# Performance work log

Hardware: AMD Instinct MI355X
Metric: run time of the kernel (lower is better)

The kernel has to match this reference:

```python
import jax, jax.numpy as jnp
import numpy as np

D_MODEL = 1024
NUM_HEADS = 16
D_K = D_MODEL // NUM_HEADS


def setup_inputs() -> dict:
    key = jax.random.key(0)
    ks = jax.random.split(key, 11)
    B, S = 2, 2048
    scale = 1.0 / np.sqrt(D_MODEL)
    inp = {
        "q": jax.random.normal(ks[0], (B, S, D_MODEL), jnp.float32),
        "k": jax.random.normal(ks[1], (B, S, D_MODEL), jnp.float32),
        "v": jax.random.normal(ks[2], (B, S, D_MODEL), jnp.float32),
        "wq": jax.random.normal(ks[3], (D_MODEL, D_MODEL), jnp.float32) * scale,
        "bq": jax.random.normal(ks[4], (D_MODEL,), jnp.float32) * 0.01,
        "wk": jax.random.normal(ks[5], (D_MODEL, D_MODEL), jnp.float32) * scale,
        "bk": jax.random.normal(ks[6], (D_MODEL,), jnp.float32) * 0.01,
        "wv": jax.random.normal(ks[7], (D_MODEL, D_MODEL), jnp.float32) * scale,
        "bv": jax.random.normal(ks[8], (D_MODEL,), jnp.float32) * 0.01,
        "wo": jax.random.normal(ks[9], (D_MODEL, D_MODEL), jnp.float32) * scale,
        "bo": jax.random.normal(ks[10], (D_MODEL,), jnp.float32) * 0.01,
    }
    return inp


def reference(q, k, v, wq, bq, wk, bk, wv, bv, wo, bo):
    B, S, _ = q.shape
    # Linear projections (torch Linear: x @ W.T + b). Weights stored [out, in].
    qh = (q @ wq.T + bq).reshape(B, S, NUM_HEADS, D_K).transpose(0, 2, 1, 3)  # [B,H,S,dk]
    kh = (k @ wk.T + bk).reshape(B, S, NUM_HEADS, D_K).transpose(0, 2, 1, 3)
    vh = (v @ wv.T + bv).reshape(B, S, NUM_HEADS, D_K).transpose(0, 2, 1, 3)
    scores = jnp.einsum("bhqd,bhkd->bhqk", qh, kh) / jnp.sqrt(jnp.asarray(D_K, qh.dtype))
    weights = jax.nn.softmax(scores, axis=-1)
    attn = jnp.einsum("bhqk,bhkd->bhqd", weights, vh)  # [B,H,S,dk]
    attn = attn.transpose(0, 2, 1, 3).reshape(B, S, D_MODEL)
    return attn @ wo.T + bo
```

## Files before the change

### kernel.cpp

```cpp
#include <hip/hip_runtime.h>

#define DM 1024
#define NH 16
#define DK 64
#define BB 2
#define SS 2048
#define MT (BB*SS)

typedef __attribute__((ext_vector_type(8))) short bf16x8;
typedef __attribute__((ext_vector_type(4))) float f32x4;

#define QSCALE 0.1803368801111191f
#define EXPC  (-14.426950408889634f)

__device__ __forceinline__ unsigned short f2bf(float f) {
    unsigned int u = __float_as_uint(f);
    u += 0x7FFF + ((u >> 16) & 1);
    return (unsigned short)(u >> 16);
}

__device__ __forceinline__ unsigned int cvt_pk_bf16(float lo, float hi) {
    unsigned int r;
    asm("v_cvt_pk_bf16_f32 %0, %1, %2" : "=v"(r) : "v"(lo), "v"(hi));
    return r;
}

__device__ __forceinline__ void gload16(const void* g, void* l) {
    __builtin_amdgcn_global_load_lds(
        (const __attribute__((address_space(1))) unsigned int*)g,
        (__attribute__((address_space(3))) unsigned int*)(unsigned int)(unsigned long long)l,
        16, 0, 0);
}

__device__ __forceinline__ int kperm(int s) {
    return (s & ~31) | (((s >> 2) & 1) << 4) | (((s >> 3) & 3) << 2) | (s & 3);
}

struct CvtArgs {
    const float* s[4];
    unsigned short* d[4];
    float scl[4];
};

__global__ __launch_bounds__(256) void cvt_f32_bf16(CvtArgs a) {
    const int arr = blockIdx.y;
    const int i = (blockIdx.x * 256 + threadIdx.x) * 8;
    const float sc = a.scl[arr];
    const float4* sp = (const float4*)(a.s[arr] + i);
    float4 x = sp[0], y = sp[1];
    union { unsigned short us[8]; uint4 u4; } r;
    r.us[0] = f2bf(x.x * sc); r.us[1] = f2bf(x.y * sc);
    r.us[2] = f2bf(x.z * sc); r.us[3] = f2bf(x.w * sc);
    r.us[4] = f2bf(y.x * sc); r.us[5] = f2bf(y.y * sc);
    r.us[6] = f2bf(y.z * sc); r.us[7] = f2bf(y.w * sc);
    *(uint4*)(a.d[arr] + i) = r.u4;
}

struct ProjArgs {
    const void* A[3];
    const void* B[3];
    const float* bias[3];
    unsigned short* out[3];
    float bscale[3];
};

__global__ __launch_bounds__(256, 3) void proj3(ProjArgs pa) {
    __shared__ __align__(16) unsigned short As[2][128 * 32];
    __shared__ __align__(16) unsigned short Bs[2][128 * 32];

    const int z = blockIdx.y;
    const int bx = blockIdx.x;
    const int xcd = bx & 7, ib = bx >> 3;
    int mb, nb;
    if (z < 2) { mb = xcd * 4 + (ib >> 3); nb = ib & 7; }
    else       { mb = ib >> 2;             nb = xcd * 4 + (ib & 3); }
    const int m0 = mb * 128, n0 = nb * 128;

    const bool a32 = (z < 2);
    const float* Fsrc = (const float*)(a32 ? pa.A[z] : pa.B[z]);
    const unsigned short* Gsrc = (const unsigned short*)(a32 ? pa.B[z] : pa.A[z]);
    const int f0r = a32 ? m0 : n0;
    const int g0r = a32 ? n0 : m0;
    unsigned short* const Fb[2] = { a32 ? As[0] : Bs[0], a32 ? As[1] : Bs[1] };
    unsigned short* const Gb[2] = { a32 ? Bs[0] : As[0], a32 ? Bs[1] : As[1] };

    const float* bias = pa.bias[z];
    const float bsc = pa.bscale[z];
    unsigned short* out = pa.out[z];

    const int tid = (int)threadIdx.x;
    const int l = tid & 63;
    const int w = tid >> 6;
    const int wm = w >> 1, wn = w & 1;

    const int strow = l >> 2;
    const int sslot = (l & 3) ^ ((l >> 3) & 3);
    const int fr = l & 15, fj = l >> 4;
    const int swz = ((fj ^ ((fr >> 1) & 3)) << 4);

    const f32x4 zero = {0.f, 0.f, 0.f, 0.f};
    f32x4 acc[4][4];
    #pragma unroll
    for (int mf = 0; mf < 4; ++mf)
        #pragma unroll
        for (int nf = 0; nf < 4; ++nf) acc[mf][nf] = zero;

    float4 r0[2][2], r1[2][2];

    #pragma unroll
    for (int t = 0; t < 2; ++t) {
        const int c = w * 2 + t;
        const int row = c * 16 + strow;
        const int col = sslot * 8;
        const float4* s = (const float4*)(Fsrc + (size_t)(f0r + row) * DM + col);
        float4 f0v = s[0], f1v = s[1];
        union { unsigned int u[4]; bf16x8 v; } pk;
        pk.u[0] = cvt_pk_bf16(f0v.x, f0v.y); pk.u[1] = cvt_pk_bf16(f0v.z, f0v.w);
        pk.u[2] = cvt_pk_bf16(f1v.x, f1v.y); pk.u[3] = cvt_pk_bf16(f1v.z, f1v.w);
        *(bf16x8*)((char*)Fb[0] + c * 1024 + l * 16) = pk.v;
        gload16(Gsrc + (size_t)(g0r + row) * DM + col, (char*)Gb[0] + c * 1024);
    }
    #pragma unroll
    for (int t = 0; t < 2; ++t) {
        const int row = (w * 2 + t) * 16 + strow;
        const float4* s = (const float4*)(Fsrc + (size_t)(f0r + row) * DM + 32 + sslot * 8);
        r0[t][0] = s[0]; r0[t][1] = s[1];
    }
    __syncthreads();

    auto body = [&](int k, int cb, float4 (&rin)[2][2], float4 (&rout)[2][2]) {
        if (k + 64 < DM) {
            #pragma unroll
            for (int t = 0; t < 2; ++t) {
                const int row = (w * 2 + t) * 16 + strow;
                const float4* s = (const float4*)(Fsrc + (size_t)(f0r + row) * DM + (k + 64) + sslot * 8);
                rout[t][0] = s[0]; rout[t][1] = s[1];
            }
        }
        if (k + 32 < DM) {
            #pragma unroll
            for (int t = 0; t < 2; ++t) {
                const int c = w * 2 + t;
                const int row = c * 16 + strow;
                gload16(Gsrc + (size_t)(g0r + row) * DM + (k + 32) + sslot * 8, (char*)Gb[cb ^ 1] + c * 1024);
            }
        }
        bf16x8 af[4], bfr[4];
        #pragma unroll
        for (int mf = 0; mf < 4; ++mf)
            af[mf] = *(const bf16x8*)((const char*)As[cb] + (wm * 64 + mf * 16 + fr) * 64 + swz);
        #pragma unroll
        for (int nf = 0; nf < 4; ++nf)
            bfr[nf] = *(const bf16x8*)((const char*)Bs[cb] + (wn * 64 + nf * 16 + fr) * 64 + swz);
        #pragma unroll
        for (int mf = 0; mf < 4; ++mf)
            #pragma unroll
            for (int nf = 0; nf < 4; ++nf)
                acc[mf][nf] = __builtin_amdgcn_mfma_f32_16x16x32_bf16(af[mf], bfr[nf], acc[mf][nf], 0, 0, 0);
        if (k + 32 < DM) {
            #pragma unroll
            for (int t = 0; t < 2; ++t) {
                const int c = w * 2 + t;
                union { unsigned int u[4]; bf16x8 v; } pk;
                pk.u[0] = cvt_pk_bf16(rin[t][0].x, rin[t][0].y);
                pk.u[1] = cvt_pk_bf16(rin[t][0].z, rin[t][0].w);
                pk.u[2] = cvt_pk_bf16(rin[t][1].x, rin[t][1].y);
                pk.u[3] = cvt_pk_bf16(rin[t][1].z, rin[t][1].w);
                *(bf16x8*)((char*)Fb[cb ^ 1] + c * 1024 + l * 16) = pk.v;
            }
        }
        __syncthreads();
    };

    for (int kt = 0; kt < DM; kt += 64) {
        body(kt, 0, r0, r1);
        body(kt + 32, 1, r1, r0);
    }

    #pragma unroll
    for (int nf = 0; nf < 4; ++nf) {
        const int n = n0 + wn * 64 + nf * 16 + fr;
        const float bn = (z == 2) ? 0.f : bias[n] * bsc;
        #pragma unroll
        for (int mf = 0; mf < 4; ++mf) {
            #pragma unroll
            for (int j = 0; j < 4; ++j) {
                const int m = m0 + wm * 64 + mf * 16 + fj * 4 + j;
                if (z < 2) {
                    const float val = acc[mf][nf][j] + bn;
                    int s = m & (SS - 1);
                    if (z == 1) s = kperm(s);
                    out[((size_t)((m >> 11) * NH + (n >> 6)) * SS + s) * DK + (n & 63)] = f2bf(val);
                } else {
                    const float val = acc[mf][nf][j] + bias[m];
                    out[(size_t)((n >> 11) * NH + (m >> 6)) * (SS * DK) + (size_t)(m & 63) * SS + (n & (SS - 1))] = f2bf(val);
                }
            }
        }
    }
}

__global__ __launch_bounds__(256, 2) void gemm_out(
    const unsigned short* __restrict__ A,
    const unsigned short* __restrict__ B,
    const float* __restrict__ bias,
    float* __restrict__ out)
{
    __shared__ __align__(16) unsigned short As[2][128 * 32];
    __shared__ __align__(16) unsigned short Bs[2][64 * 32];

    const int tid = (int)threadIdx.x;
    const int l = tid & 63;
    const int w = tid >> 6;
    const int wm = w >> 1, wn = w & 1;
    const int m0 = blockIdx.x * 128, n0 = blockIdx.y * 64;

    const int strow = l >> 2;
    const int sslot = (l & 3) ^ ((l >> 3) & 3);
    const int fr = l & 15, fj = l >> 4;
    const int swz = ((fj ^ ((fr >> 1) & 3)) << 4);

    const f32x4 zero = {0.f, 0.f, 0.f, 0.f};
    f32x4 acc[4][2];
    #pragma unroll
    for (int mf = 0; mf < 4; ++mf)
        #pragma unroll
        for (int nf = 0; nf < 2; ++nf) acc[mf][nf] = zero;

    #pragma unroll
    for (int t = 0; t < 2; ++t) {
        const int c = w * 2 + t;
        gload16(A + (size_t)(m0 + c * 16 + strow) * DM + sslot * 8, (char*)As[0] + c * 1024);
    }
    gload16(B + (size_t)(n0 + w * 16 + strow) * DM + sslot * 8, (char*)Bs[0] + w * 1024);
    __syncthreads();

    for (int kt = 0; kt < DM; kt += 32) {
        const int cb = (kt >> 5) & 1;
        if (kt + 32 < DM) {
            #pragma unroll
            for (int t = 0; t < 2; ++t) {
                const int c = w * 2 + t;
                gload16(A + (size_t)(m0 + c * 16 + strow) * DM + (kt + 32) + sslot * 8, (char*)As[cb ^ 1] + c * 1024);
            }
            gload16(B + (size_t)(n0 + w * 16 + strow) * DM + (kt + 32) + sslot * 8, (char*)Bs[cb ^ 1] + w * 1024);
        }
        bf16x8 af[4], bfr[2];
        #pragma unroll
        for (int mf = 0; mf < 4; ++mf)
            af[mf] = *(const bf16x8*)((const char*)As[cb] + (wm * 64 + mf * 16 + fr) * 64 + swz);
        #pragma unroll
        for (int nf = 0; nf < 2; ++nf)
            bfr[nf] = *(const bf16x8*)((const char*)Bs[cb] + (wn * 32 + nf * 16 + fr) * 64 + swz);
        #pragma unroll
        for (int mf = 0; mf < 4; ++mf)
            #pragma unroll
            for (int nf = 0; nf < 2; ++nf)
                acc[mf][nf] = __builtin_amdgcn_mfma_f32_16x16x32_bf16(af[mf], bfr[nf], acc[mf][nf], 0, 0, 0);
        __syncthreads();
    }

    #pragma unroll
    for (int nf = 0; nf < 2; ++nf) {
        const int n = n0 + wn * 32 + nf * 16 + fr;
        const float bn = bias[n];
        #pragma unroll
        for (int mf = 0; mf < 4; ++mf)
            #pragma unroll
            for (int j = 0; j < 4; ++j) {
                const int m = m0 + wm * 64 + mf * 16 + fj * 4 + j;
                out[(size_t)m * DM + n] = acc[mf][nf][j] + bn;
            }
    }
}

__global__ __launch_bounds__(256, 2) void attn_bf16(
    const unsigned short* __restrict__ qh,
    const unsigned short* __restrict__ kh,
    const unsigned short* __restrict__ vt,
    unsigned short* __restrict__ ao)
{
    __shared__ __align__(16) unsigned short Ks[2][128 * 64];
    __shared__ __align__(16) unsigned short Vs[2][2][64 * 64];

    const int tid = (int)threadIdx.x;
    const int l = tid & 63;
    const int w = tid >> 6;
    const int bh = blockIdx.x;
    const int q0 = blockIdx.y * 128;
    const size_t pb = (size_t)bh * (SS * DK);

    const int fr = l & 15, fj = l >> 4;
    const int s8 = fr & 7;
    const int strow = l >> 3;
    const int sslot = (l & 7) ^ strow;

    bf16x8 qreg[2][2];
    #pragma unroll
    for (int qf = 0; qf < 2; ++qf)
        #pragma unroll
        for (int ks = 0; ks < 2; ++ks)
            qreg[qf][ks] = *(const bf16x8*)(qh + pb + (size_t)(q0 + w * 32 + qf * 16 + fr) * DK + ks * 32 + fj * 8);

    #pragma unroll
    for (int t = 0; t < 4; ++t) {
        const int c = w * 4 + t;
        gload16(kh + pb + (size_t)(c * 8 + strow) * DK + sslot * 8, (char*)Ks[0] + c * 1024);
    }
    #pragma unroll
    for (int s = 0; s < 2; ++s)
        #pragma unroll
        for (int tt = 0; tt < 2; ++tt) {
            const int ch = w * 2 + tt;
            gload16(vt + pb + (size_t)(ch * 8 + strow) * SS + s * 64 + sslot * 8, (char*)Vs[0][s] + ch * 1024);
        }
    asm volatile("s_waitcnt vmcnt(0)" ::: "memory");
    __syncthreads();

    const f32x4 zero = {0.f, 0.f, 0.f, 0.f};
    f32x4 ot[4][2];
    f32x4 lacc[2];
    #pragma unroll
    for (int nf = 0; nf < 4; ++nf)
        #pragma unroll
        for (int qf = 0; qf < 2; ++qf) ot[nf][qf] = zero;
    lacc[0] = zero; lacc[1] = zero;

    const int NT = SS / 128;
    for (int t = 0; t < NT; ++t) {
        const int c = t & 1;
        if (t + 1 < NT) {
            #pragma unroll
            for (int t4 = 0; t4 < 4; ++t4) {
                const int ch = w * 4 + t4;
                gload16(kh + pb + (size_t)((t + 1) * 128 + ch * 8 + strow) * DK + sslot * 8,
                        (char*)Ks[c ^ 1] + ch * 1024);
            }
        }
        f32x4 sc[8][2];
        #pragma unroll
        for (int kf = 0; kf < 8; ++kf)
            #pragma unroll
            for (int qf = 0; qf < 2; ++qf) sc[kf][qf] = zero;
        __builtin_amdgcn_s_setprio(1);
        #pragma unroll
        for (int ks = 0; ks < 2; ++ks) {
            bf16x8 kfr[8];
            #pragma unroll
            for (int kf = 0; kf < 8; ++kf)
                kfr[kf] = *(const bf16x8*)((const char*)Ks[c] + (kf * 16 + fr) * 128 + (((ks * 4 + fj) ^ s8) << 4));
            #pragma unroll
            for (int kf = 0; kf < 8; ++kf)
                #pragma unroll
                for (int qf = 0; qf < 2; ++qf)
                    sc[kf][qf] = __builtin_amdgcn_mfma_f32_16x16x32_bf16(kfr[kf], qreg[qf][ks], sc[kf][qf], 0, 0, 0);
        }
        __builtin_amdgcn_s_setprio(0);

        bf16x8 pbf[2][4];
        #pragma unroll
        for (int qf = 0; qf < 2; ++qf) {
            #pragma unroll
            for (int kss = 0; kss < 4; ++kss) {
                union { unsigned int u[4]; bf16x8 v; } pk;
                #pragma unroll
                for (int kf = 0; kf < 2; ++kf) {
                    const f32x4 s4 = sc[kss * 2 + kf][qf];
                    const float e0 = __builtin_amdgcn_exp2f(s4[0] + EXPC);
                    const float e1 = __builtin_amdgcn_exp2f(s4[1] + EXPC);
                    const float e2 = __builtin_amdgcn_exp2f(s4[2] + EXPC);
                    const float e3 = __builtin_amdgcn_exp2f(s4[3] + EXPC);
                    lacc[qf][0] += e0; lacc[qf][1] += e1;
                    lacc[qf][2] += e2; lacc[qf][3] += e3;
                    pk.u[kf * 2 + 0] = cvt_pk_bf16(e0, e1);
                    pk.u[kf * 2 + 1] = cvt_pk_bf16(e2, e3);
                }
                pbf[qf][kss] = pk.v;
            }
        }

        __builtin_amdgcn_sched_barrier(0);
        asm volatile("s_waitcnt vmcnt(0) lgkmcnt(0)" ::: "memory");
        __builtin_amdgcn_s_barrier();
        __builtin_amdgcn_sched_barrier(0);

        if (t + 1 < NT) {
            #pragma unroll
            for (int s = 0; s < 2; ++s)
                #pragma unroll
                for (int tt = 0; tt < 2; ++tt) {
                    const int ch = w * 2 + tt;
                    gload16(vt + pb + (size_t)(ch * 8 + strow) * SS + (t + 1) * 128 + s * 64 + sslot * 8,
                            (char*)Vs[c ^ 1][s] + ch * 1024);
                }
        }

        __builtin_amdgcn_s_setprio(1);
        #pragma unroll
        for (int kss = 0; kss < 4; ++kss) {
            const int sub = kss >> 1, kw = kss & 1;
            bf16x8 va[4];
            #pragma unroll
            for (int nf = 0; nf < 4; ++nf)
                va[nf] = *(const bf16x8*)((const char*)Vs[c][sub] + (nf * 16 + fr) * 128 + (((kw * 4 + fj) ^ s8) << 4));
            #pragma unroll
            for (int nf = 0; nf < 4; ++nf)
                #pragma unroll
                for (int qf = 0; qf < 2; ++qf)
                    ot[nf][qf] = __builtin_amdgcn_mfma_f32_16x16x32_bf16(va[nf], pbf[qf][kss], ot[nf][qf], 0, 0, 0);
        }
        __builtin_amdgcn_s_setprio(0);
    }

    float inv[2];
    #pragma unroll
    for (int qf = 0; qf < 2; ++qf) {
        float s = (lacc[qf][0] + lacc[qf][1]) + (lacc[qf][2] + lacc[qf][3]);
        s += __shfl_xor(s, 16);
        s += __shfl_xor(s, 32);
        inv[qf] = 1.0f / s;
    }
    const int b = bh >> 4, h = bh & 15;
    #pragma unroll
    for (int qf = 0; qf < 2; ++qf) {
        const int qg = q0 + w * 32 + qf * 16 + fr;
        unsigned short* dst = ao + (size_t)(b * SS + qg) * DM + h * DK + fj * 4;
        #pragma unroll
        for (int nf = 0; nf < 4; ++nf) {
            uint2 pw;
            pw.x = cvt_pk_bf16(ot[nf][qf][0] * inv[qf], ot[nf][qf][1] * inv[qf]);
            pw.y = cvt_pk_bf16(ot[nf][qf][2] * inv[qf], ot[nf][qf][3] * inv[qf]);
            *(uint2*)(dst + nf * 16) = pw;
        }
    }
}

extern "C" void kernel_launch(void* const* d_in, const int* in_sizes, int n_in,
                              void* d_out, int out_size, void* d_ws, size_t ws_size,
                              hipStream_t stream) {
    const float* q  = (const float*)d_in[0];
    const float* k  = (const float*)d_in[1];
    const float* v  = (const float*)d_in[2];
    const float* wq = (const float*)d_in[3];
    const float* bq = (const float*)d_in[4];
    const float* wk = (const float*)d_in[5];
    const float* bk = (const float*)d_in[6];
    const float* wv = (const float*)d_in[7];
    const float* bv = (const float*)d_in[8];
    const float* wo = (const float*)d_in[9];
    const float* bo = (const float*)d_in[10];

    const size_t NQ = (size_t)MT * DM;
    const size_t NW = (size_t)DM * DM;
    unsigned short* wsb = (unsigned short*)d_ws;
    unsigned short* wqb = wsb;
    unsigned short* wkb = wqb + NW;
    unsigned short* wvb = wkb + NW;
    unsigned short* wob = wvb + NW;
    unsigned short* qhb = wob + NW;
    unsigned short* khb = qhb + NQ;
    unsigned short* vtb = khb + NQ;
    unsigned short* aob = vtb + NQ;

    CvtArgs ca;
    ca.s[0] = wq; ca.d[0] = wqb; ca.scl[0] = QSCALE;
    ca.s[1] = wk; ca.d[1] = wkb; ca.scl[1] = 1.f;
    ca.s[2] = wv; ca.d[2] = wvb; ca.scl[2] = 1.f;
    ca.s[3] = wo; ca.d[3] = wob; ca.scl[3] = 1.f;
    cvt_f32_bf16<<<dim3(512, 4), dim3(256), 0, stream>>>(ca);

    ProjArgs pa;
    pa.A[0] = q;   pa.B[0] = wqb; pa.bias[0] = bq; pa.out[0] = qhb; pa.bscale[0] = QSCALE;
    pa.A[1] = k;   pa.B[1] = wkb; pa.bias[1] = bk; pa.out[1] = khb; pa.bscale[1] = 1.f;
    pa.A[2] = wvb; pa.B[2] = v;   pa.bias[2] = bv; pa.out[2] = vtb; pa.bscale[2] = 1.f;
    proj3<<<dim3(256, 3), dim3(256), 0, stream>>>(pa);

    attn_bf16<<<dim3(32, 16), dim3(256), 0, stream>>>(qhb, khb, vtb, aob);

    gemm_out<<<dim3(32, 16), dim3(256), 0, stream>>>(aob, wob, bo, (float*)d_out);
}
```

Baseline: 112.7 us.

## Triple-buffer direct-to-LDS bf16 operand loads in proj3 with explicit vmcnt waits

The projection GEMM now keeps the bf16 operand, loaded directly into LDS, in a three-stage ring and issues its load two k-steps ahead instead of one. __syncthreads is replaced by an explicit s_waitcnt vmcnt plus s_barrier, so in-flight global loads for later stages are not drained at each barrier. The aim is to hide global memory latency. In exchange LDS use per block grows from 32KB to 40KB, which may reduce occupancy at launch_bounds 3, and the hand-counted vmcnt values are fragile.

```diff
diff --git a/kernel.cpp b/kernel.cpp
--- a/kernel.cpp
+++ b/kernel.cpp
@@ -65,8 +65,8 @@
 };
 
 __global__ __launch_bounds__(256, 3) void proj3(ProjArgs pa) {
-    __shared__ __align__(16) unsigned short As[2][128 * 32];
-    __shared__ __align__(16) unsigned short Bs[2][128 * 32];
+    __shared__ __align__(16) unsigned short Fb[2][128 * 32];
+    __shared__ __align__(16) unsigned short Gr[3][128 * 32];
 
     const int z = blockIdx.y;
     const int bx = blockIdx.x;
@@ -81,8 +81,6 @@
     const unsigned short* Gsrc = (const unsigned short*)(a32 ? pa.B[z] : pa.A[z]);
     const int f0r = a32 ? m0 : n0;
     const int g0r = a32 ? n0 : m0;
-    unsigned short* const Fb[2] = { a32 ? As[0] : Bs[0], a32 ? As[1] : Bs[1] };
-    unsigned short* const Gb[2] = { a32 ? Bs[0] : As[0], a32 ? Bs[1] : As[1] };
 
     const float* bias = pa.bias[z];
     const float bsc = pa.bscale[z];
@@ -107,18 +105,34 @@
 
     float4 r0[2][2], r1[2][2];
 
+    float4 f0v[2][2];
+    #pragma unroll
+    for (int t = 0; t < 2; ++t) {
+        const int row = (w * 2 + t) * 16 + strow;
+        const float4* s = (const float4*)(Fsrc + (size_t)(f0r + row) * DM + sslot * 8);
+        f0v[t][0] = s[0]; f0v[t][1] = s[1];
+    }
     #pragma unroll
     for (int t = 0; t < 2; ++t) {
         const int c = w * 2 + t;
         const int row = c * 16 + strow;
-        const int col = sslot * 8;
-        const float4* s = (const float4*)(Fsrc + (size_t)(f0r + row) * DM + col);
-        float4 f0v = s[0], f1v = s[1];
+        gload16(Gsrc + (size_t)(g0r + row) * DM + sslot * 8, (char*)Gr[0] + c * 1024);
+    }
+    #pragma unroll
+    for (int t = 0; t < 2; ++t) {
+        const int c = w * 2 + t;
+        const int row = c * 16 + strow;
+        gload16(Gsrc + (size_t)(g0r + row) * DM + 32 + sslot * 8, (char*)Gr[1] + c * 1024);
+    }
+    #pragma unroll
+    for (int t = 0; t < 2; ++t) {
+        const int c = w * 2 + t;
         union { unsigned int u[4]; bf16x8 v; } pk;
-        pk.u[0] = cvt_pk_bf16(f0v.x, f0v.y); pk.u[1] = cvt_pk_bf16(f0v.z, f0v.w);
-        pk.u[2] = cvt_pk_bf16(f1v.x, f1v.y); pk.u[3] = cvt_pk_bf16(f1v.z, f1v.w);
+        pk.u[0] = cvt_pk_bf16(f0v[t][0].x, f0v[t][0].y);
+        pk.u[1] = cvt_pk_bf16(f0v[t][0].z, f0v[t][0].w);
+        pk.u[2] = cvt_pk_bf16(f0v[t][1].x, f0v[t][1].y);
+        pk.u[3] = cvt_pk_bf16(f0v[t][1].z, f0v[t][1].w);
         *(bf16x8*)((char*)Fb[0] + c * 1024 + l * 16) = pk.v;
-        gload16(Gsrc + (size_t)(g0r + row) * DM + col, (char*)Gb[0] + c * 1024);
     }
     #pragma unroll
     for (int t = 0; t < 2; ++t) {
@@ -126,38 +140,46 @@
         const float4* s = (const float4*)(Fsrc + (size_t)(f0r + row) * DM + 32 + sslot * 8);
         r0[t][0] = s[0]; r0[t][1] = s[1];
     }
-    __syncthreads();
-
-    auto body = [&](int k, int cb, float4 (&rin)[2][2], float4 (&rout)[2][2]) {
-        if (k + 64 < DM) {
+    __builtin_amdgcn_sched_barrier(0);
+    asm volatile("s_waitcnt vmcnt(4) lgkmcnt(0)" ::: "memory");
+    __builtin_amdgcn_s_barrier();
+    __builtin_amdgcn_sched_barrier(0);
+
+    auto body = [&](int k, int cb, int gcur, int giss,
+                    float4 (&rin)[2][2], float4 (&rout)[2][2]) {
+        const bool pf64 = (k + 64 < DM);
+        const bool pf32 = (k + 32 < DM);
+        if (pf64) {
             #pragma unroll
             for (int t = 0; t < 2; ++t) {
                 const int row = (w * 2 + t) * 16 + strow;
                 const float4* s = (const float4*)(Fsrc + (size_t)(f0r + row) * DM + (k + 64) + sslot * 8);
                 rout[t][0] = s[0]; rout[t][1] = s[1];
             }
-        }
-        if (k + 32 < DM) {
             #pragma unroll
             for (int t = 0; t < 2; ++t) {
                 const int c = w * 2 + t;
                 const int row = c * 16 + strow;
-                gload16(Gsrc + (size_t)(g0r + row) * DM + (k + 32) + sslot * 8, (char*)Gb[cb ^ 1] + c * 1024);
-            }
-        }
+                gload16(Gsrc + (size_t)(g0r + row) * DM + (k + 64) + sslot * 8,
+                        (char*)Gr[0] + giss * 8192 + c * 1024);
+            }
+        }
+        const char* GLds = (const char*)Gr[0] + gcur * 8192;
+        const char* ALds = a32 ? (const char*)Fb[cb] : GLds;
+        const char* BLds = a32 ? GLds : (const char*)Fb[cb];
         bf16x8 af[4], bfr[4];
         #pragma unroll
         for (int mf = 0; mf < 4; ++mf)
-            af[mf] = *(const bf16x8*)((const char*)As[cb] + (wm * 64 + mf * 16 + fr) * 64 + swz);
+            af[mf] = *(const bf16x8*)(ALds + (wm * 64 + mf * 16 + fr) * 64 + swz);
         #pragma unroll
         for (int nf = 0; nf < 4; ++nf)
-            bfr[nf] = *(const bf16x8*)((const char*)Bs[cb] + (wn * 64 + nf * 16 + fr) * 64 + swz);
+            bfr[nf] = *(const bf16x8*)(BLds + (wn * 64 + nf * 16 + fr) * 64 + swz);
         #pragma unroll
         for (int mf = 0; mf < 4; ++mf)
             #pragma unroll
             for (int nf = 0; nf < 4; ++nf)
                 acc[mf][nf] = __builtin_amdgcn_mfma_f32_16x16x32_bf16(af[mf], bfr[nf], acc[mf][nf], 0, 0, 0);
-        if (k + 32 < DM) {
+        if (pf32) {
             #pragma unroll
             for (int t = 0; t < 2; ++t) {
                 const int c = w * 2 + t;
@@ -169,12 +191,18 @@
                 *(bf16x8*)((char*)Fb[cb ^ 1] + c * 1024 + l * 16) = pk.v;
             }
         }
-        __syncthreads();
+        __builtin_amdgcn_sched_barrier(0);
+        if (pf64) asm volatile("s_waitcnt vmcnt(6) lgkmcnt(0)" ::: "memory");
+        else      asm volatile("s_waitcnt vmcnt(0) lgkmcnt(0)" ::: "memory");
+        __builtin_amdgcn_s_barrier();
+        __builtin_amdgcn_sched_barrier(0);
     };
 
+    int s = 0;
     for (int kt = 0; kt < DM; kt += 64) {
-        body(kt, 0, r0, r1);
-        body(kt + 32, 1, r1, r0);
+        body(kt,      0, s,           (s + 2) % 3, r0, r1);
+        body(kt + 32, 1, (s + 1) % 3, s,           r1, r0);
+        s = (s + 2) % 3;
     }
 
     #pragma unroll
@@ -188,9 +216,9 @@
                 const int m = m0 + wm * 64 + mf * 16 + fj * 4 + j;
                 if (z < 2) {
                     const float val = acc[mf][nf][j] + bn;
-                    int s = m & (SS - 1);
-                    if (z == 1) s = kperm(s);
-                    out[((size_t)((m >> 11) * NH + (n >> 6)) * SS + s) * DK + (n & 63)] = f2bf(val);
+                    int ss = m & (SS - 1);
+                    if (z == 1) ss = kperm(ss);
+                    out[((size_t)((m >> 11) * NH + (n >> 6)) * SS + ss) * DK + (n & 63)] = f2bf(val);
                 } else {
                     const float val = acc[mf][nf][j] + bias[m];
                     out[(size_t)((n >> 11) * NH + (m >> 6)) * (SS * DK) + (size_t)(m & 63) * SS + (n & (SS - 1))] = f2bf(val);
```

Result: no change. 113.1 us (+0.4%).
